# Performance work log

Measured on AMD Instinct MI355X. Metric: run time of the kernel, lower is better.

## Reference

```python
import jax, jax.numpy as jnp
import numpy as np

SEQ_LEN, BATCH, T = 128, 32, 32
START, END = 30, 31  # start_tag / end_tag from init_kwargs


def setup_inputs() -> dict:
    key = jax.random.key(0)
    k1, k2 = jax.random.split(key)
    scores = jax.random.normal(k1, (SEQ_LEN, BATCH, T, T, T), dtype=jnp.float32)
    target = jax.random.randint(k2, (SEQ_LEN, BATCH, 1), 0, T ** 3, dtype=jnp.int64)
    mask = jnp.ones((SEQ_LEN, BATCH), dtype=bool)
    return {"scores": scores, "target": target, "mask": mask}


def reference(scores, target, mask):
    seq_len, bat = scores.shape[0], scores.shape[1]

    # gold-path energy: gather flattened tag-triple score at each step, masked sum
    flat = scores.reshape(seq_len, bat, -1)                  # (S, B, T^3)
    tg = jnp.take_along_axis(flat, target, axis=2)[..., 0]   # (S, B)
    tg_energy = jnp.sum(jnp.where(mask, tg, jnp.zeros((), tg.dtype)))

    # init partition over (prev_prev=START fixed out) -> (B, T, T) over (prev, cur)
    p1 = scores[0, :, START, START, :]                       # (B, T)
    partition = p1[:, :, None] + scores[1, :, START, :, :]   # (B, T, T)

    # forward-algorithm recurrence: logsumexp out oldest tag each step
    def step(part, inp):
        s_t, m_t = inp                                       # (B,T,T,T), (B,)
        cur = s_t + part[:, :, :, None]                      # broadcast over new tag
        cp = jax.nn.logsumexp(cur, axis=1)                   # (B, T, T)
        part = jnp.where(m_t[:, None, None], cp, part)
        return part, None

    partition, _ = jax.lax.scan(step, partition, (scores[2:], mask[2:]))

    z = partition[:, END, END].sum()
    return (z - tg_energy) / bat  # average_batch=True
```

## Files before the change

kernel.cpp:

```cpp
#include <hip/hip_runtime.h>
#include <hip/hip_bf16.h>
#include <math.h>

#define SEQ_LEN 128
#define BATCH   32
#define T       32
#define TT      (T*T)
#define TTT     (T*T*T)
#define START   30
#define END     31

#define LOG2E   1.44269504088896f
#define OFF4    5.77078016355587f

typedef unsigned long long u64;

__device__ __forceinline__ u64 pt_pack(int tag, float v) {
    union { float f; unsigned int u; } c; c.f = v;
    return ((u64)(unsigned int)tag << 32) | (u64)c.u;
}
__device__ __forceinline__ float pt_val(u64 w) {
    union { unsigned int u; float f; } c; c.u = (unsigned int)w; return c.f;
}
__device__ __forceinline__ int pt_tag(u64 w) { return (int)(w >> 32); }

__device__ __forceinline__ u64 ald64(const u64* p) {
    return __hip_atomic_load(p, __ATOMIC_RELAXED, __HIP_MEMORY_SCOPE_AGENT);
}
__device__ __forceinline__ void ast64(u64* p, u64 v) {
    __hip_atomic_store(p, v, __ATOMIC_RELAXED, __HIP_MEMORY_SCOPE_AGENT);
}

#define BLOCK_SYNC() do {                                   \
    asm volatile("s_waitcnt lgkmcnt(0)" ::: "memory");      \
    __builtin_amdgcn_sched_barrier(0);                      \
    __builtin_amdgcn_s_barrier();                           \
    __builtin_amdgcn_sched_barrier(0);                      \
} while (0)

__global__ __launch_bounds__(256) void tg_kernel(const float* __restrict__ scores,
                                                 const int*   __restrict__ target,
                                                 const int*   __restrict__ mask,
                                                 float*       __restrict__ ws) {
    int idx = blockIdx.x * 256 + threadIdx.x;
    float v = 0.0f;
    if (mask[idx] != 0) v = scores[(size_t)idx * TTT + target[idx]];
    #pragma unroll
    for (int off = 32; off > 0; off >>= 1) v += __shfl_down(v, off, 64);
    __shared__ float partial[4];
    int wave = threadIdx.x >> 6, lane = threadIdx.x & 63;
    if (lane == 0) partial[wave] = v;
    __syncthreads();
    if (threadIdx.x == 0)
        ws[blockIdx.x] = partial[0] + partial[1] + partial[2] + partial[3];
}

__global__ __launch_bounds__(256) void init_dfb(const float* __restrict__ scores,
                                                u64* __restrict__ ptF,
                                                u64* __restrict__ ptB) {
    const int blk = blockIdx.x, tid = threadIdx.x;
    if (blk < BATCH) {
        const int b = blk;
        u64* pt = ptF + (size_t)b * 2048;
        #pragma unroll
        for (int q = 0; q < 4; ++q) {
            int e = q * 256 + tid;
            int i = e & 31, j = e >> 5;
            float p1 = scores[(size_t)(0*BATCH + b)*TTT + START*TT + START*T + i];
            float s1 = scores[(size_t)(1*BATCH + b)*TTT + START*TT + i*T + j];
            pt[1024 + e] = pt_pack(1, __expf(p1 + s1));
            pt[e]        = 0ULL;
        }
    } else {
        const int b = blk - BATCH;
        u64* pt = ptB + (size_t)b * 2048;
        #pragma unroll
        for (int q = 0; q < 4; ++q) {
            int e = q * 256 + tid;
            float v = (e == END*T + END) ? 1.0f : 0.0f;
            pt[e]        = pt_pack(128, v);
            pt[1024 + e] = 0ULL;
        }
    }
}

__global__ __launch_bounds__(512, 4) void scan_dfb(const float* __restrict__ scores,
                                                   const int*   __restrict__ maskI,
                                                   u64*         __restrict__ ptF,
                                                   u64*         __restrict__ ptB) {
    const int bid   = blockIdx.x;
    const int g     = bid & 7;
    const int chain = bid >> 3;
    const int b     = chain & 31;
    const bool dirB = (chain >> 5) != 0;
    const int tid   = threadIdx.x;
    const int lane  = tid & 63;

    __shared__ float smem[128 * 33];
    __shared__ float pld[128];
    __shared__ float res[128];
    __shared__ int   lmask[SEQ_LEN];

    if (tid < SEQ_LEN) lmask[tid] = maskI[tid * BATCH + b];
    __syncthreads();

    u64* const pt = (dirB ? ptB : ptF) + (size_t)b * 2048;

    const int i0 = tid >> 5;
    const int f  = tid & 31;
    const size_t offA = (size_t)i0 * TT + g * 128 + f * 4;

    const int jjB = (tid & 31) >> 3;
    const int k4  = tid & 7;
    const int oF  = tid >> 2;
    const int s4  = tid & 3;
    const int jjF = oF >> 5;

    float4 SA0, SA1, SB0, SB1;

    auto T_of = [&](int s) { return dirB ? (127 - s) : (2 + s); };

    auto issue = [&](float4& X0, float4& X1, int t) {
        const float* p = scores + ((size_t)t * BATCH + b) * TTT;
        X0 = *(const float4*)(p + offA);
        X1 = *(const float4*)(p + offA + 16 * TT);
    };

    auto addr_of = [&](int o) -> int {
        return dirB ? ((o >> 2) * 32 + 4 * g + (o & 3))
                    : ((o & 31) * 32 + 4 * g + (o >> 5));
    };

    auto step = [&](float4& X0, float4& X1, int t) {
        const bool act   = (lmask[t] != 0);
        const int srcpar = dirB ? ((t + 1) & 1) : ((t - 1) & 1);
        const int tagw   = dirB ? (t + 1) : (t - 1);

        if (!dirB && act) {
            #pragma unroll
            for (int q = 0; q < 4; ++q) smem[(f*4 + q)*33 + i0]        = (&X0.x)[q];
            #pragma unroll
            for (int q = 0; q < 4; ++q) smem[(f*4 + q)*33 + (i0 + 16)] = (&X1.x)[q];
        }

        if (tid < 64) {
            if (act) {
                const u64* src = pt + (size_t)srcpar * 1024 + 128 * g;
                u64 wv0 = 0, wv1 = 0; bool d0 = false, d1 = false;
                while (true) {
                    if (!d0) { wv0 = ald64(src + lane);      d0 = (pt_tag(wv0) == tagw); }
                    if (!d1) { wv1 = ald64(src + 64 + lane); d1 = (pt_tag(wv1) == tagw); }
                    if (__all(d0 && d1)) break;
                }
                pld[lane]      = pt_val(wv0);
                pld[lane + 64] = pt_val(wv1);
            } else {
                const u64* base = pt + (size_t)srcpar * 1024;
                const int o0 = lane, o1 = lane + 64;
                const int a0 = addr_of(o0), a1 = addr_of(o1);
                u64 x0 = 0, x1 = 0; bool d0 = false, d1 = false;
                while (true) {
                    if (!d0) { x0 = ald64(base + a0); d0 = (pt_tag(x0) == tagw); }
                    if (!d1) { x1 = ald64(base + a1); d1 = (pt_tag(x1) == tagw); }
                    if (__all(d0 && d1)) break;
                }
                pld[o0] = pt_val(x0);
                pld[o1] = pt_val(x1);
            }
        }
        BLOCK_SYNC();

        if (act) {
            if (!dirB) {
                float acc = 0.f;
                #pragma unroll
                for (int m = 0; m < 8; ++m) {
                    const int i = s4*8 + m;
                    float E = exp2f(fmaf(smem[oF*33 + i], LOG2E, -OFF4));
                    acc = fmaf(E, pld[jjF*32 + i], acc);
                }
                acc += __shfl_xor(acc, 1, 64);
                acc += __shfl_xor(acc, 2, 64);
                if (s4 == 0) res[oF] = acc;
            } else {
                const float4 Rv = *(const float4*)&pld[jjB*32 + k4*4];
                float acc0, acc1;
                {
                    float e0 = exp2f(fmaf(X0.x, LOG2E, -OFF4));
                    float e1 = exp2f(fmaf(X0.y, LOG2E, -OFF4));
                    float e2 = exp2f(fmaf(X0.z, LOG2E, -OFF4));
                    float e3 = exp2f(fmaf(X0.w, LOG2E, -OFF4));
                    acc0 = fmaf(e3, Rv.w, fmaf(e2, Rv.z, fmaf(e1, Rv.y, e0 * Rv.x)));
                }
                {
                    float e0 = exp2f(fmaf(X1.x, LOG2E, -OFF4));
                    float e1 = exp2f(fmaf(X1.y, LOG2E, -OFF4));
                    float e2 = exp2f(fmaf(X1.z, LOG2E, -OFF4));
                    float e3 = exp2f(fmaf(X1.w, LOG2E, -OFF4));
                    acc1 = fmaf(e3, Rv.w, fmaf(e2, Rv.z, fmaf(e1, Rv.y, e0 * Rv.x)));
                }
                acc0 += __shfl_xor(acc0, 1, 64);
                acc0 += __shfl_xor(acc0, 2, 64);
                acc0 += __shfl_xor(acc0, 4, 64);
                acc1 += __shfl_xor(acc1, 1, 64);
                acc1 += __shfl_xor(acc1, 2, 64);
                acc1 += __shfl_xor(acc1, 4, 64);
                if (k4 == 0) {
                    res[i0*4 + jjB]        = acc0;
                    res[(i0 + 16)*4 + jjB] = acc1;
                }
            }
        }
        BLOCK_SYNC();

        if (tid < 64) {
            const int o0 = lane, o1 = lane + 64;
            const float v0 = act ? res[o0] : pld[o0];
            const float v1 = act ? res[o1] : pld[o1];
            u64* dst = pt + (size_t)(t & 1) * 1024;
            ast64(dst + addr_of(o0), pt_pack(t, v0));
            ast64(dst + addr_of(o1), pt_pack(t, v1));
        }
    };

    issue(SA0, SA1, T_of(0));
    for (int s = 0; s < 63; s += 2) {
        if (s + 1 < 63) issue(SB0, SB1, T_of(s + 1));
        step(SA0, SA1, T_of(s));
        if (s + 1 < 63) {
            if (s + 2 < 63) issue(SA0, SA1, T_of(s + 2));
            step(SB0, SB1, T_of(s + 1));
        }
    }
}

__global__ __launch_bounds__(1024) void finalize_dfb(const float* __restrict__ ws,
                                                     const u64*  __restrict__ ptF,
                                                     const u64*  __restrict__ ptB,
                                                     const int*  __restrict__ mask,
                                                     float*      __restrict__ out) {
    __shared__ float zs[32];
    const int w = threadIdx.x >> 6, lane = threadIdx.x & 63;
    for (int rep = 0; rep < 2; ++rep) {
        const int b = w + rep * 16;
        const u64* qf = ptF + (size_t)b * 2048;
        const u64* rb = ptB + (size_t)b * 2048 + 1024;
        float dot = 0.f;
        #pragma unroll
        for (int e = 0; e < 16; ++e) {
            const int x = lane + 64 * e;
            dot += pt_val(qf[x]) * pt_val(rb[(x & 31) * 32 + (x >> 5)]);
        }
        float cnt = 0.f;
        {
            int t = 2 + lane;
            if (t < SEQ_LEN) cnt += (mask[t*BATCH + b] != 0) ? 1.f : 0.f;
            t += 64;
            if (t < SEQ_LEN) cnt += (mask[t*BATCH + b] != 0) ? 1.f : 0.f;
        }
        #pragma unroll
        for (int off = 32; off > 0; off >>= 1) {
            dot += __shfl_xor(dot, off, 64);
            cnt += __shfl_xor(cnt, off, 64);
        }
        if (lane == 0) zs[b] = 4.0f * cnt + logf(dot);
    }
    __syncthreads();
    if (threadIdx.x == 0) {
        float tg = 0.f, z = 0.f;
        #pragma unroll
        for (int i = 0; i < 16; ++i) tg += ws[i];
        #pragma unroll
        for (int i = 0; i < 32; ++i) z += zs[i];
        out[0] = (z - tg) / (float)BATCH;
    }
}

__global__ __launch_bounds__(1024) void scan_fast(const float* __restrict__ scores,
                                                  const int*   __restrict__ maskI,
                                                  float*       __restrict__ ws) {
    const int b    = blockIdx.x;
    const int tid  = threadIdx.x;
    const int w    = tid >> 6;
    const int lane = tid & 63;
    const int h    = lane >> 4;
    const int jp   = (lane >> 3) & 1;
    const int k4   = lane & 7;
    const int j    = w * 2 + jp;

    __shared__ float Q[2][TT];
    __shared__ int   lmask[SEQ_LEN];
    if (tid < SEQ_LEN) lmask[tid] = maskI[tid * BATCH + b];
    {
        int x = tid >> 5, y = tid & 31;
        float p1 = scores[(size_t)(0*BATCH + b)*TTT + START*TT + START*T + x];
        float s1 = scores[(size_t)(1*BATCH + b)*TTT + START*TT + x*T + y];
        Q[1][x*T + y] = __expf(p1 + s1);
    }
    __syncthreads();
    const int loff = h*8*TT + j*T + k4*4;
    float4 SA[8], SB[8];
    auto issue = [&](float4 (&S)[8], int t) {
        const float* p = scores + ((size_t)t*BATCH + b)*TTT + loff;
        #pragma unroll
        for (int m = 0; m < 8; ++m) S[m] = *(const float4*)(p + m*TT);
    };
    auto process = [&](float4 (&S)[8], int t) {
        const float* qc = Q[(t-1) & 1];
        float*       qn = Q[t & 1];
        #pragma unroll
        for (int m = 0; m < 8; ++m) {
            S[m].x = exp2f(fmaf(S[m].x, LOG2E, -OFF4));
            S[m].y = exp2f(fmaf(S[m].y, LOG2E, -OFF4));
            S[m].z = exp2f(fmaf(S[m].z, LOG2E, -OFF4));
            S[m].w = exp2f(fmaf(S[m].w, LOG2E, -OFF4));
        }
        float4 acc = make_float4(0.f, 0.f, 0.f, 0.f);
        #pragma unroll
        for (int m = 0; m < 8; ++m) {
            float q = qc[(h*8 + m)*T + j];
            acc.x = fmaf(S[m].x, q, acc.x);
            acc.y = fmaf(S[m].y, q, acc.y);
            acc.z = fmaf(S[m].z, q, acc.z);
            acc.w = fmaf(S[m].w, q, acc.w);
        }
        acc.x += __shfl_xor(acc.x, 16, 64); acc.y += __shfl_xor(acc.y, 16, 64);
        acc.z += __shfl_xor(acc.z, 16, 64); acc.w += __shfl_xor(acc.w, 16, 64);
        acc.x += __shfl_xor(acc.x, 32, 64); acc.y += __shfl_xor(acc.y, 32, 64);
        acc.z += __shfl_xor(acc.z, 32, 64); acc.w += __shfl_xor(acc.w, 32, 64);
        if (lane < 16) {
            if (lmask[t] != 0) *(float4*)&qn[j*T + k4*4] = acc;
            else               *(float4*)&qn[j*T + k4*4] = *(const float4*)&qc[j*T + k4*4];
        }
        BLOCK_SYNC();
    };
    issue(SA, 2);
    for (int t = 2; t < SEQ_LEN; t += 2) {
        issue(SB, t + 1);
        process(SA, t);
        if (t + 2 < SEQ_LEN) issue(SA, t + 2);
        process(SB, t + 1);
    }
    if (tid == 0) {
        int cnt = 0;
        for (int t = 2; t < SEQ_LEN; ++t) cnt += (lmask[t] != 0);
        ws[16 + b] = 4.0f * (float)cnt + logf(Q[1][END*T + END]);
    }
}

__global__ void finalize_simple(const float* __restrict__ ws, float* __restrict__ out) {
    if (threadIdx.x == 0) {
        float tg = 0.f, z = 0.f;
        #pragma unroll
        for (int i = 0; i < 16; ++i) tg += ws[i];
        #pragma unroll
        for (int i = 0; i < 32; ++i) z += ws[16 + i];
        out[0] = (z - tg) / (float)BATCH;
    }
}

extern "C" void kernel_launch(void* const* d_in, const int* in_sizes, int n_in,
                              void* d_out, int out_size, void* d_ws, size_t ws_size,
                              hipStream_t stream) {
    const float* scores = (const float*)d_in[0];
    const int*   target = (const int*)d_in[1];
    const int*   mask   = (const int*)d_in[2];
    float* out = (float*)d_out;
    float* ws  = (float*)d_ws;
    u64*   ptF = (u64*)((char*)d_ws + 1024);
    u64*   ptB = ptF + (size_t)BATCH * 2048;
    const size_t need = 1024 + (size_t)2 * BATCH * 2048 * sizeof(u64);

    tg_kernel<<<16, 256, 0, stream>>>(scores, target, mask, ws);
    if (ws_size >= need) {
        init_dfb<<<2*BATCH, 256, 0, stream>>>(scores, ptF, ptB);
        scan_dfb<<<512, 512, 0, stream>>>(scores, mask, ptF, ptB);
        finalize_dfb<<<1, 1024, 0, stream>>>(ws, ptF, ptB, mask, out);
    } else {
        scan_fast<<<BATCH, 1024, 0, stream>>>(scores, mask, ws);
        finalize_simple<<<1, 64, 0, stream>>>(ws, out);
    }
}
```

Baseline: 187.7 us.

## Restructure split-direction scan to one barrier per step with owner-written partitions

```diff
diff --git a/kernel.cpp b/kernel.cpp
--- a/kernel.cpp
+++ b/kernel.cpp
@@ -84,10 +84,10 @@
     }
 }
 
-__global__ __launch_bounds__(512, 4) void scan_dfb(const float* __restrict__ scores,
-                                                   const int*   __restrict__ maskI,
-                                                   u64*         __restrict__ ptF,
-                                                   u64*         __restrict__ ptB) {
+__global__ __launch_bounds__(512, 4) void scan_rd(const float* __restrict__ scores,
+                                                  const int*   __restrict__ maskI,
+                                                  u64*         __restrict__ ptF,
+                                                  u64*         __restrict__ ptB) {
     const int bid   = blockIdx.x;
     const int g     = bid & 7;
     const int chain = bid >> 3;
@@ -96,140 +96,141 @@
     const int tid   = threadIdx.x;
     const int lane  = tid & 63;
 
-    __shared__ float smem[128 * 33];
-    __shared__ float pld[128];
-    __shared__ float res[128];
-    __shared__ int   lmask[SEQ_LEN];
-
-    if (tid < SEQ_LEN) lmask[tid] = maskI[tid * BATCH + b];
-    __syncthreads();
+    const u64 mlo = __ballot(maskI[lane * BATCH + b] != 0);
+    const u64 mhi = __ballot(maskI[(64 + lane) * BATCH + b] != 0);
+    auto act_of = [&](int t) {
+        return (((t < 64) ? (mlo >> t) : (mhi >> (t - 64))) & 1ULL) != 0ULL;
+    };
 
     u64* const pt = (dirB ? ptB : ptF) + (size_t)b * 2048;
-
     const int i0 = tid >> 5;
     const int f  = tid & 31;
     const size_t offA = (size_t)i0 * TT + g * 128 + f * 4;
-
-    const int jjB = (tid & 31) >> 3;
-    const int k4  = tid & 7;
-    const int oF  = tid >> 2;
-    const int s4  = tid & 3;
-    const int jjF = oF >> 5;
-
-    float4 SA0, SA1, SB0, SB1;
-
-    auto T_of = [&](int s) { return dirB ? (127 - s) : (2 + s); };
-
-    auto issue = [&](float4& X0, float4& X1, int t) {
-        const float* p = scores + ((size_t)t * BATCH + b) * TTT;
-        X0 = *(const float4*)(p + offA);
-        X1 = *(const float4*)(p + offA + 16 * TT);
-    };
-
-    auto addr_of = [&](int o) -> int {
-        return dirB ? ((o >> 2) * 32 + 4 * g + (o & 3))
-                    : ((o & 31) * 32 + 4 * g + (o >> 5));
-    };
-
-    auto step = [&](float4& X0, float4& X1, int t) {
-        const bool act   = (lmask[t] != 0);
-        const int srcpar = dirB ? ((t + 1) & 1) : ((t - 1) & 1);
-        const int tagw   = dirB ? (t + 1) : (t - 1);
-
-        if (!dirB && act) {
+    auto sb = [&](int t) { return scores + ((size_t)t * BATCH + b) * TTT; };
+
+    if (!dirB) {
+        __shared__ __align__(16) float sm[4][128 * 33];
+        __shared__ __align__(16) float pld[2][128];
+        const int oF = tid >> 2, s4 = tid & 3;
+        const int jj = oF >> 5, k = oF & 31;
+        const int jcol = 4 * g + jj;
+        const int ownW = k * 32 + jcol;
+        float lastval = pt_val(pt[1024 + ownW]);
+
+        float4 X0, X1;
+        auto issue = [&](int t) {
+            const float* p = sb(t) + offA;
+            X0 = *(const float4*)p; X1 = *(const float4*)(p + 16 * TT);
+        };
+        auto scat = [&](int bf) {
             #pragma unroll
-            for (int q = 0; q < 4; ++q) smem[(f*4 + q)*33 + i0]        = (&X0.x)[q];
-            #pragma unroll
-            for (int q = 0; q < 4; ++q) smem[(f*4 + q)*33 + (i0 + 16)] = (&X1.x)[q];
-        }
-
-        if (tid < 64) {
-            if (act) {
-                const u64* src = pt + (size_t)srcpar * 1024 + 128 * g;
-                u64 wv0 = 0, wv1 = 0; bool d0 = false, d1 = false;
-                while (true) {
-                    if (!d0) { wv0 = ald64(src + lane);      d0 = (pt_tag(wv0) == tagw); }
-                    if (!d1) { wv1 = ald64(src + 64 + lane); d1 = (pt_tag(wv1) == tagw); }
+            for (int q = 0; q < 4; ++q) {
+                sm[bf][(f*4 + q)*33 + i0]      = (&X0.x)[q];
+                sm[bf][(f*4 + q)*33 + i0 + 16] = (&X1.x)[q];
+            }
+        };
+
+        issue(2); scat(2);
+        issue(3); scat(3);
+        issue(4);
+        __syncthreads();
+
+        for (int t = 2; t <= 64; ++t) {
+            const bool act  = act_of(t);
+            const int  pbuf = t & 1;
+            if (t + 2 <= 64) scat((t + 2) & 3);
+            if (t + 3 <= 64) issue(t + 3);
+            if (tid < 64) {
+                const int tagw = t - 1;
+                const u64* src = pt + (size_t)((t - 1) & 1) * 1024 + 128 * g;
+                u64 w0, w1; bool d0 = false, d1 = false;
+                for (;;) {
+                    if (!d0) { w0 = ald64(src + lane);      d0 = pt_tag(w0) == tagw; }
+                    if (!d1) { w1 = ald64(src + 64 + lane); d1 = pt_tag(w1) == tagw; }
                     if (__all(d0 && d1)) break;
                 }
-                pld[lane]      = pt_val(wv0);
-                pld[lane + 64] = pt_val(wv1);
+                pld[pbuf][lane]      = pt_val(w0);
+                pld[pbuf][lane + 64] = pt_val(w1);
+            }
+            BLOCK_SYNC();
+            u64* dst = pt + (size_t)(t & 1) * 1024;
+            if (act) {
+                const float* row = &sm[t & 3][oF * 33 + 8 * s4];
+                const float* pp  = &pld[pbuf][jj * 32 + 8 * s4];
+                float acc = 0.f;
+                #pragma unroll
+                for (int m = 0; m < 8; ++m)
+                    acc = fmaf(exp2f(fmaf(row[m], LOG2E, -OFF4)), pp[m], acc);
+                acc += __shfl_xor(acc, 1, 64);
+                acc += __shfl_xor(acc, 2, 64);
+                if (s4 == 0) { lastval = acc; ast64(dst + ownW, pt_pack(t, acc)); }
             } else {
-                const u64* base = pt + (size_t)srcpar * 1024;
-                const int o0 = lane, o1 = lane + 64;
-                const int a0 = addr_of(o0), a1 = addr_of(o1);
-                u64 x0 = 0, x1 = 0; bool d0 = false, d1 = false;
-                while (true) {
-                    if (!d0) { x0 = ald64(base + a0); d0 = (pt_tag(x0) == tagw); }
-                    if (!d1) { x1 = ald64(base + a1); d1 = (pt_tag(x1) == tagw); }
+                if (s4 == 0) ast64(dst + ownW, pt_pack(t, lastval));
+            }
+        }
+    } else {
+        __shared__ __align__(16) float pld[2][128];
+        const int jj = f >> 3, k4 = f & 7;
+        const int jb = 4 * g + jj;
+        const int ownW0 = i0 * 32 + jb, ownW1 = (i0 + 16) * 32 + jb;
+        float last0 = pt_val(pt[ownW0]);
+        float last1 = pt_val(pt[ownW1]);
+
+        float4 A0, A1, B0, B1;
+        auto issueR = [&](float4& Y0, float4& Y1, int t) {
+            const float* p = sb(t) + offA;
+            Y0 = *(const float4*)p; Y1 = *(const float4*)(p + 16 * TT);
+        };
+
+        auto stepB = [&](int t, const float4& X0, const float4& X1) {
+            const bool act  = act_of(t);
+            const int  pbuf = t & 1;
+            if (tid < 64) {
+                const int tagw = t + 1;
+                const u64* src = pt + (size_t)((t + 1) & 1) * 1024 + 128 * g;
+                u64 w0, w1; bool d0 = false, d1 = false;
+                for (;;) {
+                    if (!d0) { w0 = ald64(src + lane);      d0 = pt_tag(w0) == tagw; }
+                    if (!d1) { w1 = ald64(src + 64 + lane); d1 = pt_tag(w1) == tagw; }
                     if (__all(d0 && d1)) break;
                 }
-                pld[o0] = pt_val(x0);
-                pld[o1] = pt_val(x1);
-            }
-        }
-        BLOCK_SYNC();
-
-        if (act) {
-            if (!dirB) {
-                float acc = 0.f;
-                #pragma unroll
-                for (int m = 0; m < 8; ++m) {
-                    const int i = s4*8 + m;
-                    float E = exp2f(fmaf(smem[oF*33 + i], LOG2E, -OFF4));
-                    acc = fmaf(E, pld[jjF*32 + i], acc);
+                pld[pbuf][lane]      = pt_val(w0);
+                pld[pbuf][lane + 64] = pt_val(w1);
+            }
+            BLOCK_SYNC();
+            u64* dst = pt + (size_t)(t & 1) * 1024;
+            if (act) {
+                const float4 Rv = *(const float4*)&pld[pbuf][jj * 32 + 4 * k4];
+                float a0, a1;
+                a0 = exp2f(fmaf(X0.x, LOG2E, -OFF4)) * Rv.x;
+                a0 = fmaf(exp2f(fmaf(X0.y, LOG2E, -OFF4)), Rv.y, a0);
+                a0 = fmaf(exp2f(fmaf(X0.z, LOG2E, -OFF4)), Rv.z, a0);
+                a0 = fmaf(exp2f(fmaf(X0.w, LOG2E, -OFF4)), Rv.w, a0);
+                a1 = exp2f(fmaf(X1.x, LOG2E, -OFF4)) * Rv.x;
+                a1 = fmaf(exp2f(fmaf(X1.y, LOG2E, -OFF4)), Rv.y, a1);
+                a1 = fmaf(exp2f(fmaf(X1.z, LOG2E, -OFF4)), Rv.z, a1);
+                a1 = fmaf(exp2f(fmaf(X1.w, LOG2E, -OFF4)), Rv.w, a1);
+                a0 += __shfl_xor(a0, 1, 64); a0 += __shfl_xor(a0, 2, 64); a0 += __shfl_xor(a0, 4, 64);
+                a1 += __shfl_xor(a1, 1, 64); a1 += __shfl_xor(a1, 2, 64); a1 += __shfl_xor(a1, 4, 64);
+                if (k4 == 0) {
+                    last0 = a0; last1 = a1;
+                    ast64(dst + ownW0, pt_pack(t, a0));
+                    ast64(dst + ownW1, pt_pack(t, a1));
                 }
-                acc += __shfl_xor(acc, 1, 64);
-                acc += __shfl_xor(acc, 2, 64);
-                if (s4 == 0) res[oF] = acc;
             } else {
-                const float4 Rv = *(const float4*)&pld[jjB*32 + k4*4];
-                float acc0, acc1;
-                {
-                    float e0 = exp2f(fmaf(X0.x, LOG2E, -OFF4));
-                    float e1 = exp2f(fmaf(X0.y, LOG2E, -OFF4));
-                    float e2 = exp2f(fmaf(X0.z, LOG2E, -OFF4));
-                    float e3 = exp2f(fmaf(X0.w, LOG2E, -OFF4));
-                    acc0 = fmaf(e3, Rv.w, fmaf(e2, Rv.z, fmaf(e1, Rv.y, e0 * Rv.x)));
+                if (k4 == 0) {
+                    ast64(dst + ownW0, pt_pack(t, last0));
+                    ast64(dst + ownW1, pt_pack(t, last1));
                 }
-                {
-                    float e0 = exp2f(fmaf(X1.x, LOG2E, -OFF4));
-                    float e1 = exp2f(fmaf(X1.y, LOG2E, -OFF4));
-                    float e2 = exp2f(fmaf(X1.z, LOG2E, -OFF4));
-                    float e3 = exp2f(fmaf(X1.w, LOG2E, -OFF4));
-                    acc1 = fmaf(e3, Rv.w, fmaf(e2, Rv.z, fmaf(e1, Rv.y, e0 * Rv.x)));
-                }
-                acc0 += __shfl_xor(acc0, 1, 64);
-                acc0 += __shfl_xor(acc0, 2, 64);
-                acc0 += __shfl_xor(acc0, 4, 64);
-                acc1 += __shfl_xor(acc1, 1, 64);
-                acc1 += __shfl_xor(acc1, 2, 64);
-                acc1 += __shfl_xor(acc1, 4, 64);
-                if (k4 == 0) {
-                    res[i0*4 + jjB]        = acc0;
-                    res[(i0 + 16)*4 + jjB] = acc1;
-                }
-            }
-        }
-        BLOCK_SYNC();
-
-        if (tid < 64) {
-            const int o0 = lane, o1 = lane + 64;
-            const float v0 = act ? res[o0] : pld[o0];
-            const float v1 = act ? res[o1] : pld[o1];
-            u64* dst = pt + (size_t)(t & 1) * 1024;
-            ast64(dst + addr_of(o0), pt_pack(t, v0));
-            ast64(dst + addr_of(o1), pt_pack(t, v1));
-        }
-    };
-
-    issue(SA0, SA1, T_of(0));
-    for (int s = 0; s < 63; s += 2) {
-        if (s + 1 < 63) issue(SB0, SB1, T_of(s + 1));
-        step(SA0, SA1, T_of(s));
-        if (s + 1 < 63) {
-            if (s + 2 < 63) issue(SA0, SA1, T_of(s + 2));
-            step(SB0, SB1, T_of(s + 1));
+            }
+        };
+
+        issueR(A0, A1, 127);
+        for (int t = 127; t >= 65; t -= 2) {
+            if (t - 1 >= 65) issueR(B0, B1, t - 1);
+            stepB(t, A0, A1);
+            if (t - 2 >= 65) issueR(A0, A1, t - 2);
+            if (t - 1 >= 65) stepB(t - 1, B0, B1);
         }
     }
 }
@@ -332,7 +333,8 @@
             if (lmask[t] != 0) *(float4*)&qn[j*T + k4*4] = acc;
             else               *(float4*)&qn[j*T + k4*4] = *(const float4*)&qc[j*T + k4*4];
         }
-        BLOCK_SYNC();
+        asm volatile("s_waitcnt lgkmcnt(0)" ::: "memory");
+        __builtin_amdgcn_s_barrier();
     };
     issue(SA, 2);
     for (int t = 2; t < SEQ_LEN; t += 2) {
@@ -374,7 +376,7 @@
     tg_kernel<<<16, 256, 0, stream>>>(scores, target, mask, ws);
     if (ws_size >= need) {
         init_dfb<<<2*BATCH, 256, 0, stream>>>(scores, ptF, ptB);
-        scan_dfb<<<512, 512, 0, stream>>>(scores, mask, ptF, ptB);
+        scan_rd<<<512, 512, 0, stream>>>(scores, mask, ptF, ptB);
         finalize_dfb<<<1, 1024, 0, stream>>>(ws, ptF, ptB, mask, out);
     } else {
         scan_fast<<<BATCH, 1024, 0, stream>>>(scores, mask, ws);
```

Result: no change. 185.6 us (-1.1%).
